# Performance work log

Measured on AMD Instinct MI355X. Metric: run time of the kernel, lower is better.

Reference implementation:

```python
import jax, jax.numpy as jnp
import numpy as np

B, U1, U2 = 4, 2048, 2048
C = 256      # in_feat_dim
F = 256      # feat_dim
M = 4        # num_modes
D = C // M   # attention_mode_dim = 64
ATTN_CLIP = 500.0
LN_EPS = 1e-12


def setup_inputs() -> dict:
    key = jax.random.key(0)
    ks = jax.random.split(key, 8)
    s = 0.02  # base_initializer_range
    inp = {
        "query_feat": jax.random.normal(ks[0], (B, U1, C), jnp.float32),
        "key_feat": jax.random.normal(ks[1], (B, U2, C), jnp.float32),
        "Wq": jax.random.normal(ks[2], (M * D, C), jnp.float32) * s,
        "bq": jnp.zeros((M * D,), jnp.float32),
    }
    # tie_qk_scheme='shared': key linear shares query weights
    inp["Wk"] = inp["Wq"]
    inp["bk"] = inp["bq"]
    inp["Wv"] = jax.random.normal(ks[3], (M * F, C), jnp.float32) * s  # first_linear, v_has_bias=False
    inp["W_mid"] = jax.random.normal(ks[4], (F, F), jnp.float32) * s   # MMSharedMid shared_linear
    inp["b_mid"] = jnp.zeros((F,), jnp.float32)
    inp["W_out"] = jax.random.normal(ks[5], (M, F, F), jnp.float32) * s  # grouped 1x1 conv, per mode
    inp["b_out"] = jnp.zeros((M, F), jnp.float32)
    inp["ln_g"] = jnp.ones((F,), jnp.float32)   # resout LayerNorm
    inp["ln_b"] = jnp.zeros((F,), jnp.float32)
    inp["W_score"] = jax.random.normal(ks[6], (1, F), jnp.float32) * s  # LearnedSoftAggregate
    inp["b_score"] = jnp.zeros((1,), jnp.float32)
    return inp


def _layer_norm(x, g, b):
    mu = jnp.mean(x, axis=-1, keepdims=True)
    var = jnp.var(x, axis=-1, keepdims=True)
    return (x - mu) * jax.lax.rsqrt(var + LN_EPS) * g + b


def reference(query_feat, key_feat, Wq, bq, Wk, bk, Wv, W_mid, b_mid,
              W_out, b_out, ln_g, ln_b, W_score, b_score):
    # --- tied-QK multi-mode attention ---
    q = (query_feat @ Wq.T + bq).reshape(B, U1, M, D)
    k = (key_feat @ Wk.T + bk).reshape(B, U2, M, D)
    scores = jnp.einsum('bimd,bjmd->bmij', q, k) / jnp.sqrt(jnp.float32(D))
    scores = jnp.clip(scores, -ATTN_CLIP, ATTN_CLIP)  # attn_clip
    probs = jax.nn.softmax(scores, axis=-1)           # [B, M, U1, U2]

    # --- ExpandedFeatTrans: value projection + fusion ---
    v = (key_feat @ Wv.T).reshape(B, U2, M, F)        # first_linear (no bias)
    fused = jnp.einsum('bmij,bjmf->bmif', probs, v)   # [B, M, U1, F]

    # MMSharedMid: shared linear over F + gelu (dropout = identity in eval)
    mid = jax.nn.gelu(fused @ W_mid.T + b_mid, approximate=False)

    # MMPrivateOutput: per-mode grouped 1x1 conv; NOTE the original code computes
    # x_comb = x + shortcut but then layer-norms x (shortcut dropped) - kept faithful.
    out = jnp.einsum('bmif,mgf->bmig', mid, W_out) + b_out[None, :, None, :]
    out = _layer_norm(out, ln_g, ln_b)                # [B, M, U1, F]

    # LearnedSoftAggregate over modes (group_dim=1, keepdim=False)
    mode_scores = out @ W_score.T + b_score           # [B, M, U1, 1]
    mode_probs = jax.nn.softmax(mode_scores, axis=1)
    return jnp.sum(out * mode_probs, axis=1)          # [B, U1, F]
```

## Files before the change

kernel.cpp:

```cpp
#include <hip/hip_runtime.h>

typedef __attribute__((ext_vector_type(8))) short short8;
typedef __attribute__((ext_vector_type(4))) float f32x4;
typedef __attribute__((ext_vector_type(16))) float f32x16;
typedef unsigned short u16t;
typedef unsigned int u32t;

#define MFMA16(a, b, c) __builtin_amdgcn_mfma_f32_16x16x32_bf16((a), (b), (c), 0, 0, 0)
#define MFMA32(a, b, c) __builtin_amdgcn_mfma_f32_32x32x16_bf16((a), (b), (c), 0, 0, 0)

__device__ __forceinline__ u16t f2bf(float f) {
  u32t u = __float_as_uint(f);
  u32t r = u + 0x7fffu + ((u >> 16) & 1u);
  return (u16t)(r >> 16);
}
__device__ __forceinline__ float bf2f(u16t b) {
  return __uint_as_float(((u32t)b) << 16);
}
__device__ __forceinline__ short8 pack8(float4 a0, float4 a1) {
  short8 r;
  r[0] = (short)f2bf(a0.x); r[1] = (short)f2bf(a0.y);
  r[2] = (short)f2bf(a0.z); r[3] = (short)f2bf(a0.w);
  r[4] = (short)f2bf(a1.x); r[5] = (short)f2bf(a1.y);
  r[6] = (short)f2bf(a1.z); r[7] = (short)f2bf(a1.w);
  return r;
}
__device__ __forceinline__ u32t packrhu(float a, float b) {
  u32t ua = __float_as_uint(a) + 0x8000u;
  u32t ub = __float_as_uint(b) + 0x8000u;
  return (ua >> 16) | (ub & 0xffff0000u);
}

__device__ __forceinline__ void proj_dev(
    const float* __restrict__ A, const float* __restrict__ W,
    const float* __restrict__ bias, float scale,
    u16t* __restrict__ out, int mode, int bx, int by,
    u16t* As, u16t* Ws) {
  const int tid = threadIdx.x;
  const int w = tid >> 6, lane = tid & 63, quad = lane >> 4, l15 = lane & 15;
  const int l31 = lane & 31, h8 = (lane >> 5) * 8;
  const int rt = bx * 64;
  const int ct = by * 64;
  const int wrow = (w >> 1) * 32, wcol = (w & 1) * 32;
  const int r2 = tid >> 3, c8 = tid & 7;

  const f32x4 fzero = {0.f, 0.f, 0.f, 0.f};
  f32x4 acc[2][2];
#pragma unroll
  for (int i = 0; i < 2; i++)
#pragma unroll
    for (int j = 0; j < 2; j++) acc[i][j] = fzero;

  for (int kt = 0; kt < 4; ++kt) {
    __syncthreads();
#pragma unroll
    for (int hh = 0; hh < 2; ++hh) {
      int rr = r2 + hh * 32;
      const float4* pa = (const float4*)(A + (size_t)(rt + rr) * 256 + kt * 64 + c8 * 8);
      const float4* pw = (const float4*)(W + (size_t)(ct + rr) * 256 + kt * 64 + c8 * 8);
      float4 w0 = pw[0], w1 = pw[1];
      w0.x *= scale; w0.y *= scale; w0.z *= scale; w0.w *= scale;
      w1.x *= scale; w1.y *= scale; w1.z *= scale; w1.w *= scale;
      *(short8*)&As[rr * 72 + c8 * 8] = pack8(pa[0], pa[1]);
      *(short8*)&Ws[rr * 72 + c8 * 8] = pack8(w0, w1);
    }
    __syncthreads();
#pragma unroll
    for (int ks = 0; ks < 2; ++ks) {
      short8 af0 = *(const short8*)&As[(wrow + l15) * 72 + ks * 32 + quad * 8];
      short8 af1 = *(const short8*)&As[(wrow + 16 + l15) * 72 + ks * 32 + quad * 8];
      short8 bw0 = *(const short8*)&Ws[(wcol + l15) * 72 + ks * 32 + quad * 8];
      short8 bw1 = *(const short8*)&Ws[(wcol + 16 + l15) * 72 + ks * 32 + quad * 8];
      acc[0][0] = MFMA16(af0, bw0, acc[0][0]);
      acc[0][1] = MFMA16(af0, bw1, acc[0][1]);
      acc[1][0] = MFMA16(af1, bw0, acc[1][0]);
      acc[1][1] = MFMA16(af1, bw1, acc[1][1]);
    }
  }

  __syncthreads();
  u16t* Cs = As;
  if (mode == 0) {
#pragma unroll
    for (int i = 0; i < 2; i++) {
      int rl = wrow + i * 16 + quad * 4;
#pragma unroll
      for (int j = 0; j < 2; j++) {
        int cl = wcol + j * 16 + l15;
        float bv = bias ? bias[ct + cl] * scale : 0.f;
#pragma unroll
        for (int rg = 0; rg < 4; ++rg)
          Cs[(rl + rg) * 72 + cl] = f2bf(acc[i][j][rg] + bv);
      }
    }
  } else {
#pragma unroll
    for (int i = 0; i < 2; i++) {
      int rl = wrow + i * 16 + quad * 4;
#pragma unroll
      for (int j = 0; j < 2; j++) {
        int cl = wcol + j * 16 + l15;
        ushort4 pk;
        pk.x = f2bf(acc[i][j][0]);
        pk.y = f2bf(acc[i][j][1]);
        pk.z = f2bf(acc[i][j][2]);
        pk.w = f2bf(acc[i][j][3]);
        *(ushort4*)&Cs[cl * 72 + rl] = pk;
      }
    }
  }
  __syncthreads();

#pragma unroll
  for (int t2 = 0; t2 < 2; ++t2) {
    short8 frag = *(const short8*)&Cs[(t2 * 32 + l31) * 72 + w * 16 + h8];
    size_t base;
    if (mode == 0) {
      int b = rt >> 11, m = by;
      int it32 = ((rt & 2047) >> 5) + t2;
      base = (((size_t)(b * 4 + m) * 64 + it32) * 4 + w) * 512;
    } else {
      int b = rt >> 11, m = by >> 2;
      int fb = ((by & 3) << 1) + t2;
      int jt16 = ((rt & 2047) >> 4) + w;
      base = (((size_t)(b * 4 + m) * 8 + fb) * 128 + jt16) * 512;
    }
    *(short8*)(out + base + lane * 8) = frag;
  }
}

__global__ __launch_bounds__(256) void prep_kernel(
    const float* __restrict__ query, const float* __restrict__ key,
    const float* __restrict__ Wq, const float* __restrict__ bq,
    const float* __restrict__ Wv, const float* __restrict__ Wm,
    const float* __restrict__ Wo,
    u16t* __restrict__ WmB, u16t* __restrict__ WoB,
    u16t* __restrict__ QfB, u16t* __restrict__ KfB, u16t* __restrict__ VfB) {
  __shared__ __align__(16) u16t As[64 * 72];
  __shared__ __align__(16) u16t Ws[64 * 72];
  const int blk = blockIdx.x;
  const int tid = threadIdx.x;
  if (blk < 256) {
    int i = blk * 256 + tid;
    WmB[i] = f2bf(Wm[i]);
    return;
  }
  if (blk < 1280) {
    int i = (blk - 256) * 256 + tid;
    WoB[i] = f2bf(Wo[i]);
    return;
  }
  const float *A, *W, *bias;
  float scale;
  u16t* out;
  int mode, local;
  if (blk < 1792) {
    local = blk - 1280; A = query; W = Wq; bias = bq; scale = 0.125f; out = QfB; mode = 0;
  } else if (blk < 2304) {
    local = blk - 1792; A = key; W = Wq; bias = bq; scale = 1.0f; out = KfB; mode = 0;
  } else {
    local = blk - 2304; A = key; W = Wv; bias = nullptr; scale = 1.0f; out = VfB; mode = 1;
  }
  proj_dev(A, W, bias, scale, out, mode, local & 127, local >> 7, As, Ws);
}

__global__ __launch_bounds__(256, 3) void attn_kernel(
    const u16t* __restrict__ Qf, const u16t* __restrict__ Kf,
    const u16t* __restrict__ Vf,
    const u16t* __restrict__ Wmid, const u16t* __restrict__ Wout,
    const float* __restrict__ b_mid, const float* __restrict__ b_out,
    const float* __restrict__ ln_g, const float* __restrict__ ln_b,
    const float* __restrict__ Wsc, const float* __restrict__ b_sc,
    u16t* __restrict__ out_ln, float* __restrict__ scoresWS) {
  __shared__ __align__(16) u16t smBig[16640];
  __shared__ float smL[128];
  __shared__ float smR[128];
  __shared__ float smS[64];
  const int tid = threadIdx.x;
  const int w = tid >> 6, lane = tid & 63, quad = lane >> 4, l15 = lane & 15;
  const int l31 = lane & 31, h = lane >> 5;
  const int L = blockIdx.x;
  const int xcd = L & 7, slot = L >> 3;
  const int bm = xcd * 2 + (slot >> 6);
  const int it32 = slot & 63;
  const int m = bm & 3;
  const int q0 = it32 * 32;

  const size_t lane8 = (size_t)lane * 8;

  const u16t* qbase = Qf + ((size_t)(bm * 64 + it32) * 4) * 512 + lane8;
  short8 qf4[4];
#pragma unroll
  for (int ksd = 0; ksd < 4; ++ksd)
    qf4[ksd] = *(const short8*)(qbase + ksd * 512);

  const u16t* kbase = Kf + ((size_t)bm * 256) * 512 + lane8;
  const u16t* vbase = Vf + ((size_t)(bm * 8 + 2 * w) * 128) * 512 + lane8;

  f32x16 facc[2];
#pragma unroll
  for (int j = 0; j < 2; j++)
#pragma unroll
    for (int r = 0; r < 16; r++) facc[j][r] = 0.f;
  float lsum = 0.f;

  short8 kfA[4], kfB[4];
#pragma unroll
  for (int ksd = 0; ksd < 4; ++ksd) {
    kfA[ksd] = *(const short8*)(kbase + (size_t)w * 2048 + ksd * 512);
    kfB[ksd] = *(const short8*)(kbase + (size_t)(w + 4) * 2048 + ksd * 512);
  }

#pragma unroll 1
  for (int t = 0; t < 8; ++t) {
    u16t* Pb = &smBig[(t & 1) * 8320];
    f32x16 saccA, saccB;
#pragma unroll
    for (int r = 0; r < 16; r++) { saccA[r] = 0.f; saccB[r] = 0.f; }
#pragma unroll
    for (int ksd = 0; ksd < 4; ++ksd) {
      saccA = MFMA32(kfA[ksd], qf4[ksd], saccA);
      saccB = MFMA32(kfB[ksd], qf4[ksd], saccB);
    }

    float ls = 0.f;
#pragma unroll
    for (int tt = 0; tt < 8; ++tt) {
      const int jl = ((2 * tt) & 3) + 8 * ((2 * tt) >> 2) + 4 * h;
      float a0 = __expf(saccA[2 * tt]);
      float a1 = __expf(saccA[2 * tt + 1]);
      float b0 = __expf(saccB[2 * tt]);
      float b1 = __expf(saccB[2 * tt + 1]);
      ls += a0 + a1 + b0 + b1;
      *(u32t*)&Pb[l31 * 260 + w * 32 + jl] = packrhu(a0, a1);
      *(u32t*)&Pb[l31 * 260 + (w + 4) * 32 + jl] = packrhu(b0, b1);
    }
    lsum += ls;

    __syncthreads();

    if (t < 7) {
      const int jA = (t + 1) * 8 + w, jB = jA + 4;
#pragma unroll
      for (int ksd = 0; ksd < 4; ++ksd) {
        kfA[ksd] = *(const short8*)(kbase + (size_t)jA * 2048 + ksd * 512);
        kfB[ksd] = *(const short8*)(kbase + (size_t)jB * 2048 + ksd * 512);
      }
    }
#pragma unroll
    for (int jj = 0; jj < 8; ++jj) {
      short8 vf[2][2];
#pragma unroll
      for (int fb = 0; fb < 2; ++fb)
#pragma unroll
        for (int ks2 = 0; ks2 < 2; ++ks2)
          vf[fb][ks2] = *(const short8*)(vbase + ((size_t)fb * 128 + (t * 16 + jj * 2 + ks2)) * 512);
      short8 bbL[2];
#pragma unroll
      for (int ks2 = 0; ks2 < 2; ++ks2)
        bbL[ks2] = *(const short8*)&Pb[l31 * 260 + jj * 32 + ks2 * 16 + h * 8];
      facc[0] = MFMA32(vf[0][0], bbL[0], facc[0]);
      facc[0] = MFMA32(vf[0][1], bbL[1], facc[0]);
      facc[1] = MFMA32(vf[1][0], bbL[0], facc[1]);
      facc[1] = MFMA32(vf[1][1], bbL[1], facc[1]);
    }
  }

  lsum += __shfl_xor(lsum, 32);
  if (h == 0) smL[w * 32 + l31] = lsum;
  __syncthreads();
  float inv = 1.f / (smL[l31] + smL[32 + l31] + smL[64 + l31] + smL[96 + l31]);

  u16t* smF = smBig;
#pragma unroll
  for (int fb = 0; fb < 2; ++fb) {
#pragma unroll
    for (int g = 0; g < 4; ++g) {
      int fbase = w * 64 + fb * 32 + 8 * g + 4 * h;
      ushort4 pk4;
      pk4.x = f2bf(facc[fb][4 * g + 0] * inv);
      pk4.y = f2bf(facc[fb][4 * g + 1] * inv);
      pk4.z = f2bf(facc[fb][4 * g + 2] * inv);
      pk4.w = f2bf(facc[fb][4 * g + 3] * inv);
      *(ushort4*)&smF[l31 * 264 + fbase] = pk4;
    }
  }
  __syncthreads();

  const int rgrp = w >> 1, ch = w & 1;
  const int rowq = rgrp * 16 + quad * 4;
  const f32x4 fz4 = {0.f, 0.f, 0.f, 0.f};

  f32x4 macc[8];
#pragma unroll
  for (int i = 0; i < 8; i++) macc[i] = fz4;
  for (int kc = 0; kc < 8; ++kc) {
    short8 af = *(const short8*)&smF[(rgrp * 16 + l15) * 264 + kc * 32 + quad * 8];
#pragma unroll
    for (int nb = 0; nb < 8; ++nb) {
      short8 bw = *(const short8*)(Wmid + (size_t)(ch * 128 + nb * 16 + l15) * 256 + kc * 32 + quad * 8);
      macc[nb] = MFMA16(af, bw, macc[nb]);
    }
  }
#pragma unroll
  for (int nb = 0; nb < 8; ++nb) {
    int c = ch * 128 + nb * 16 + l15;
    float bmv = b_mid[c];
#pragma unroll
    for (int rg = 0; rg < 4; ++rg) {
      float x = macc[nb][rg] + bmv;
      macc[nb][rg] = 0.5f * x * (1.f + erff(x * 0.70710678118654752f));
    }
  }
  __syncthreads();
#pragma unroll
  for (int nb = 0; nb < 8; ++nb)
#pragma unroll
    for (int rg = 0; rg < 4; ++rg)
      smF[(rowq + rg) * 264 + ch * 128 + nb * 16 + l15] = f2bf(macc[nb][rg]);
  __syncthreads();

  const u16t* Wo = Wout + (size_t)m * 65536;
  f32x4 oacc[8];
#pragma unroll
  for (int i = 0; i < 8; i++) oacc[i] = fz4;
  for (int kc = 0; kc < 8; ++kc) {
    short8 af = *(const short8*)&smF[(rgrp * 16 + l15) * 264 + kc * 32 + quad * 8];
#pragma unroll
    for (int nb = 0; nb < 8; ++nb) {
      short8 bw = *(const short8*)(Wo + (size_t)(ch * 128 + nb * 16 + l15) * 256 + kc * 32 + quad * 8);
      oacc[nb] = MFMA16(af, bw, oacc[nb]);
    }
  }

  float sum[4] = {0, 0, 0, 0}, sq[4] = {0, 0, 0, 0};
#pragma unroll
  for (int nb = 0; nb < 8; ++nb) {
    int c = ch * 128 + nb * 16 + l15;
    float bo = b_out[m * 256 + c];
#pragma unroll
    for (int rg = 0; rg < 4; ++rg) {
      float x = oacc[nb][rg] + bo;
      oacc[nb][rg] = x;
      sum[rg] += x;
      sq[rg] += x * x;
    }
  }
#pragma unroll
  for (int rg = 0; rg < 4; ++rg) {
    float s = sum[rg], s2 = sq[rg];
    s += __shfl_xor(s, 1); s += __shfl_xor(s, 2); s += __shfl_xor(s, 4); s += __shfl_xor(s, 8);
    s2 += __shfl_xor(s2, 1); s2 += __shfl_xor(s2, 2); s2 += __shfl_xor(s2, 4); s2 += __shfl_xor(s2, 8);
    if (l15 == 0) {
      smR[(rowq + rg) + 32 * ch] = s;
      smR[64 + (rowq + rg) + 32 * ch] = s2;
    }
  }
  __syncthreads();
  float mu[4], rstd[4];
#pragma unroll
  for (int rg = 0; rg < 4; ++rg) {
    int r = rowq + rg;
    float s = smR[r] + smR[r + 32];
    float s2 = smR[64 + r] + smR[64 + r + 32];
    float mean = s * (1.f / 256.f);
    float var = s2 * (1.f / 256.f) - mean * mean;
    mu[rg] = mean;
    rstd[rg] = rsqrtf(var + 1e-12f);
  }

  float scp[4] = {0, 0, 0, 0};
#pragma unroll
  for (int nb = 0; nb < 8; ++nb) {
    int c = ch * 128 + nb * 16 + l15;
    float g = ln_g[c], bb2 = ln_b[c], wsv = Wsc[c];
#pragma unroll
    for (int rg = 0; rg < 4; ++rg) {
      float xn = (oacc[nb][rg] - mu[rg]) * rstd[rg] * g + bb2;
      out_ln[((size_t)bm * 2048 + (q0 + rowq + rg)) * 256 + c] = f2bf(xn);
      scp[rg] += xn * wsv;
    }
  }
#pragma unroll
  for (int rg = 0; rg < 4; ++rg) {
    float s = scp[rg];
    s += __shfl_xor(s, 1); s += __shfl_xor(s, 2); s += __shfl_xor(s, 4); s += __shfl_xor(s, 8);
    if (l15 == 0) smS[(rowq + rg) + 32 * ch] = s;
  }
  __syncthreads();
  if (ch == 0 && l15 == 0) {
#pragma unroll
    for (int rg = 0; rg < 4; ++rg) {
      int r = rowq + rg;
      scoresWS[bm * 2048 + q0 + r] = smS[r] + smS[r + 32] + b_sc[0];
    }
  }
}

__global__ __launch_bounds__(256) void agg_kernel(
    const u16t* __restrict__ out_ln, const float* __restrict__ scoresWS,
    float* __restrict__ out) {
  const int row = blockIdx.x;
  const int c = threadIdx.x;
  const int b = row >> 11, i = row & 2047;
  float s0 = scoresWS[(b * 4 + 0) * 2048 + i];
  float s1 = scoresWS[(b * 4 + 1) * 2048 + i];
  float s2 = scoresWS[(b * 4 + 2) * 2048 + i];
  float s3 = scoresWS[(b * 4 + 3) * 2048 + i];
  float mx = fmaxf(fmaxf(s0, s1), fmaxf(s2, s3));
  float e0 = __expf(s0 - mx), e1 = __expf(s1 - mx), e2 = __expf(s2 - mx), e3 = __expf(s3 - mx);
  float inv = 1.f / (e0 + e1 + e2 + e3);
  float acc = e0 * inv * bf2f(out_ln[((size_t)(b * 4 + 0) * 2048 + i) * 256 + c]) +
              e1 * inv * bf2f(out_ln[((size_t)(b * 4 + 1) * 2048 + i) * 256 + c]) +
              e2 * inv * bf2f(out_ln[((size_t)(b * 4 + 2) * 2048 + i) * 256 + c]) +
              e3 * inv * bf2f(out_ln[((size_t)(b * 4 + 3) * 2048 + i) * 256 + c]);
  out[(size_t)row * 256 + c] = acc;
}

extern "C" void kernel_launch(void* const* d_in, const int* in_sizes, int n_in,
                              void* d_out, int out_size, void* d_ws, size_t ws_size,
                              hipStream_t stream) {
  (void)in_sizes; (void)n_in; (void)out_size; (void)ws_size;
  const float* query = (const float*)d_in[0];
  const float* key   = (const float*)d_in[1];
  const float* Wq    = (const float*)d_in[2];
  const float* bq    = (const float*)d_in[3];
  const float* Wv    = (const float*)d_in[6];
  const float* Wm    = (const float*)d_in[7];
  const float* bmid  = (const float*)d_in[8];
  const float* Wo    = (const float*)d_in[9];
  const float* bo    = (const float*)d_in[10];
  const float* lng   = (const float*)d_in[11];
  const float* lnb   = (const float*)d_in[12];
  const float* Wsc   = (const float*)d_in[13];
  const float* bsc   = (const float*)d_in[14];

  char* p = (char*)d_ws;
  u16t* QfB = (u16t*)p; p += (size_t)2097152 * 2;
  u16t* KfB = (u16t*)p; p += (size_t)2097152 * 2;
  u16t* VfB = (u16t*)p; p += (size_t)8388608 * 2;
  u16t* WmB = (u16t*)p; p += (size_t)65536 * 2;
  u16t* WoB = (u16t*)p; p += (size_t)262144 * 2;
  u16t* outLn = (u16t*)p; p += (size_t)8388608 * 2;
  float* scWS = (float*)p; p += (size_t)32768 * 4;

  prep_kernel<<<4352, 256, 0, stream>>>(query, key, Wq, bq, Wv, Wm, Wo,
                                        WmB, WoB, QfB, KfB, VfB);

  attn_kernel<<<1024, 256, 0, stream>>>(QfB, KfB, VfB, WmB, WoB,
                                        bmid, bo, lng, lnb, Wsc, bsc,
                                        outLn, scWS);

  agg_kernel<<<8192, 256, 0, stream>>>(outLn, scWS, (float*)d_out);
}
```

Before: 247.1 us.

## Double attention query tile to 64 rows per block to reuse K/V loads

Each attention block now processes 64 query rows (two 32-row sub-tiles) instead of 32, so every K and V fragment loaded from global memory feeds twice as many MFMAs. The grid is halved to 512 blocks, each with 16 key steps of 4 key blocks, and the per-sub-tile softmax sums are tracked separately. The MLP/LayerNorm tail is re-partitioned so each wave owns 16 full rows, which removes the shared-memory reductions and two barriers for row statistics and scores. The cost is more accumulator registers, since the launch-bounds occupancy hint is dropped, and only 512 blocks, which risks lower occupancy and latency hiding.

After: 281.5 us. 1.14x slower.

```diff
diff --git a/kernel.cpp b/kernel.cpp
--- a/kernel.cpp
+++ b/kernel.cpp
@@ -164,7 +164,7 @@
   proj_dev(A, W, bias, scale, out, mode, local & 127, local >> 7, As, Ws);
 }
 
-__global__ __launch_bounds__(256, 3) void attn_kernel(
+__global__ __launch_bounds__(256) void attn_kernel(
     const u16t* __restrict__ Qf, const u16t* __restrict__ Kf,
     const u16t* __restrict__ Vf,
     const u16t* __restrict__ Wmid, const u16t* __restrict__ Wout,
@@ -172,139 +172,145 @@
     const float* __restrict__ ln_g, const float* __restrict__ ln_b,
     const float* __restrict__ Wsc, const float* __restrict__ b_sc,
     u16t* __restrict__ out_ln, float* __restrict__ scoresWS) {
-  __shared__ __align__(16) u16t smBig[16640];
-  __shared__ float smL[128];
-  __shared__ float smR[128];
-  __shared__ float smS[64];
+  __shared__ __align__(16) u16t smBig[16896];
+  __shared__ float smL[256];
   const int tid = threadIdx.x;
   const int w = tid >> 6, lane = tid & 63, quad = lane >> 4, l15 = lane & 15;
   const int l31 = lane & 31, h = lane >> 5;
   const int L = blockIdx.x;
   const int xcd = L & 7, slot = L >> 3;
-  const int bm = xcd * 2 + (slot >> 6);
-  const int it32 = slot & 63;
+  const int bm = xcd * 2 + (slot >> 5);
+  const int it64 = slot & 31;
   const int m = bm & 3;
-  const int q0 = it32 * 32;
+  const int q0 = it64 * 64;
 
   const size_t lane8 = (size_t)lane * 8;
 
-  const u16t* qbase = Qf + ((size_t)(bm * 64 + it32) * 4) * 512 + lane8;
-  short8 qf4[4];
-#pragma unroll
-  for (int ksd = 0; ksd < 4; ++ksd)
-    qf4[ksd] = *(const short8*)(qbase + ksd * 512);
+  const u16t* qb0 = Qf + ((size_t)(bm * 64 + it64 * 2) * 4) * 512 + lane8;
+  short8 qf[2][4];
+#pragma unroll
+  for (int ib = 0; ib < 2; ++ib)
+#pragma unroll
+    for (int ksd = 0; ksd < 4; ++ksd)
+      qf[ib][ksd] = *(const short8*)(qb0 + ((size_t)ib * 4 + ksd) * 512);
 
   const u16t* kbase = Kf + ((size_t)bm * 256) * 512 + lane8;
   const u16t* vbase = Vf + ((size_t)(bm * 8 + 2 * w) * 128) * 512 + lane8;
 
-  f32x16 facc[2];
-#pragma unroll
-  for (int j = 0; j < 2; j++)
-#pragma unroll
-    for (int r = 0; r < 16; r++) facc[j][r] = 0.f;
-  float lsum = 0.f;
-
-  short8 kfA[4], kfB[4];
-#pragma unroll
-  for (int ksd = 0; ksd < 4; ++ksd) {
-    kfA[ksd] = *(const short8*)(kbase + (size_t)w * 2048 + ksd * 512);
-    kfB[ksd] = *(const short8*)(kbase + (size_t)(w + 4) * 2048 + ksd * 512);
-  }
+  f32x16 facc[2][2];
+#pragma unroll
+  for (int a = 0; a < 2; a++)
+#pragma unroll
+    for (int b2 = 0; b2 < 2; b2++)
+#pragma unroll
+      for (int r = 0; r < 16; r++) facc[a][b2][r] = 0.f;
+  float lsum[2] = {0.f, 0.f};
+
+  short8 kf4[4];
+#pragma unroll
+  for (int ksd = 0; ksd < 4; ++ksd)
+    kf4[ksd] = *(const short8*)(kbase + (size_t)w * 2048 + ksd * 512);
 
 #pragma unroll 1
-  for (int t = 0; t < 8; ++t) {
-    u16t* Pb = &smBig[(t & 1) * 8320];
-    f32x16 saccA, saccB;
-#pragma unroll
-    for (int r = 0; r < 16; r++) { saccA[r] = 0.f; saccB[r] = 0.f; }
-#pragma unroll
-    for (int ksd = 0; ksd < 4; ++ksd) {
-      saccA = MFMA32(kfA[ksd], qf4[ksd], saccA);
-      saccB = MFMA32(kfB[ksd], qf4[ksd], saccB);
-    }
-
-    float ls = 0.f;
-#pragma unroll
-    for (int tt = 0; tt < 8; ++tt) {
-      const int jl = ((2 * tt) & 3) + 8 * ((2 * tt) >> 2) + 4 * h;
-      float a0 = __expf(saccA[2 * tt]);
-      float a1 = __expf(saccA[2 * tt + 1]);
-      float b0 = __expf(saccB[2 * tt]);
-      float b1 = __expf(saccB[2 * tt + 1]);
-      ls += a0 + a1 + b0 + b1;
-      *(u32t*)&Pb[l31 * 260 + w * 32 + jl] = packrhu(a0, a1);
-      *(u32t*)&Pb[l31 * 260 + (w + 4) * 32 + jl] = packrhu(b0, b1);
-    }
-    lsum += ls;
+  for (int t = 0; t < 16; ++t) {
+    u16t* Pb = &smBig[(t & 1) * 8448];
+#pragma unroll
+    for (int ib = 0; ib < 2; ++ib) {
+      f32x16 sacc;
+#pragma unroll
+      for (int r = 0; r < 16; r++) sacc[r] = 0.f;
+#pragma unroll
+      for (int ksd = 0; ksd < 4; ++ksd)
+        sacc = MFMA32(kf4[ksd], qf[ib][ksd], sacc);
+      float ls = 0.f;
+#pragma unroll
+      for (int tt = 0; tt < 8; ++tt) {
+        const int jl = ((2 * tt) & 3) + 8 * ((2 * tt) >> 2) + 4 * h;
+        float p0 = __expf(sacc[2 * tt]);
+        float p1 = __expf(sacc[2 * tt + 1]);
+        ls += p0 + p1;
+        *(u32t*)&Pb[ib * 4224 + l31 * 132 + w * 32 + jl] = packrhu(p0, p1);
+      }
+      lsum[ib] += ls;
+    }
 
     __syncthreads();
 
-    if (t < 7) {
-      const int jA = (t + 1) * 8 + w, jB = jA + 4;
-#pragma unroll
-      for (int ksd = 0; ksd < 4; ++ksd) {
-        kfA[ksd] = *(const short8*)(kbase + (size_t)jA * 2048 + ksd * 512);
-        kfB[ksd] = *(const short8*)(kbase + (size_t)jB * 2048 + ksd * 512);
+    if (t < 15) {
+      const int jn = (t + 1) * 4 + w;
+#pragma unroll
+      for (int ksd = 0; ksd < 4; ++ksd)
+        kf4[ksd] = *(const short8*)(kbase + (size_t)jn * 2048 + ksd * 512);
+    }
+#pragma unroll
+    for (int jj = 0; jj < 4; ++jj) {
+      short8 vf[2][2];
+#pragma unroll
+      for (int fb = 0; fb < 2; ++fb)
+#pragma unroll
+        for (int ks2 = 0; ks2 < 2; ++ks2)
+          vf[fb][ks2] = *(const short8*)(vbase + ((size_t)fb * 128 + (t * 8 + jj * 2 + ks2)) * 512);
+#pragma unroll
+      for (int ib = 0; ib < 2; ++ib) {
+        short8 bbL[2];
+#pragma unroll
+        for (int ks2 = 0; ks2 < 2; ++ks2)
+          bbL[ks2] = *(const short8*)&Pb[ib * 4224 + l31 * 132 + jj * 32 + ks2 * 16 + h * 8];
+        facc[0][ib] = MFMA32(vf[0][0], bbL[0], facc[0][ib]);
+        facc[0][ib] = MFMA32(vf[0][1], bbL[1], facc[0][ib]);
+        facc[1][ib] = MFMA32(vf[1][0], bbL[0], facc[1][ib]);
+        facc[1][ib] = MFMA32(vf[1][1], bbL[1], facc[1][ib]);
       }
     }
-#pragma unroll
-    for (int jj = 0; jj < 8; ++jj) {
-      short8 vf[2][2];
-#pragma unroll
-      for (int fb = 0; fb < 2; ++fb)
-#pragma unroll
-        for (int ks2 = 0; ks2 < 2; ++ks2)
-          vf[fb][ks2] = *(const short8*)(vbase + ((size_t)fb * 128 + (t * 16 + jj * 2 + ks2)) * 512);
-      short8 bbL[2];
-#pragma unroll
-      for (int ks2 = 0; ks2 < 2; ++ks2)
-        bbL[ks2] = *(const short8*)&Pb[l31 * 260 + jj * 32 + ks2 * 16 + h * 8];
-      facc[0] = MFMA32(vf[0][0], bbL[0], facc[0]);
-      facc[0] = MFMA32(vf[0][1], bbL[1], facc[0]);
-      facc[1] = MFMA32(vf[1][0], bbL[0], facc[1]);
-      facc[1] = MFMA32(vf[1][1], bbL[1], facc[1]);
-    }
-  }
-
-  lsum += __shfl_xor(lsum, 32);
-  if (h == 0) smL[w * 32 + l31] = lsum;
-  __syncthreads();
-  float inv = 1.f / (smL[l31] + smL[32 + l31] + smL[64 + l31] + smL[96 + l31]);
+  }
+
+#pragma unroll
+  for (int ib = 0; ib < 2; ++ib) {
+    lsum[ib] += __shfl_xor(lsum[ib], 32);
+    if (h == 0) smL[ib * 128 + w * 32 + l31] = lsum[ib];
+  }
+  __syncthreads();
+  float inv[2];
+#pragma unroll
+  for (int ib = 0; ib < 2; ++ib)
+    inv[ib] = 1.f / (smL[ib * 128 + l31] + smL[ib * 128 + 32 + l31] +
+                     smL[ib * 128 + 64 + l31] + smL[ib * 128 + 96 + l31]);
 
   u16t* smF = smBig;
 #pragma unroll
-  for (int fb = 0; fb < 2; ++fb) {
-#pragma unroll
-    for (int g = 0; g < 4; ++g) {
-      int fbase = w * 64 + fb * 32 + 8 * g + 4 * h;
-      ushort4 pk4;
-      pk4.x = f2bf(facc[fb][4 * g + 0] * inv);
-      pk4.y = f2bf(facc[fb][4 * g + 1] * inv);
-      pk4.z = f2bf(facc[fb][4 * g + 2] * inv);
-      pk4.w = f2bf(facc[fb][4 * g + 3] * inv);
-      *(ushort4*)&smF[l31 * 264 + fbase] = pk4;
-    }
-  }
-  __syncthreads();
-
-  const int rgrp = w >> 1, ch = w & 1;
-  const int rowq = rgrp * 16 + quad * 4;
+  for (int fb = 0; fb < 2; ++fb)
+#pragma unroll
+    for (int ib = 0; ib < 2; ++ib) {
+      const int i = ib * 32 + l31;
+#pragma unroll
+      for (int g = 0; g < 4; ++g) {
+        int fbase = w * 64 + fb * 32 + 8 * g + 4 * h;
+        ushort4 pk4;
+        pk4.x = f2bf(facc[fb][ib][4 * g + 0] * inv[ib]);
+        pk4.y = f2bf(facc[fb][ib][4 * g + 1] * inv[ib]);
+        pk4.z = f2bf(facc[fb][ib][4 * g + 2] * inv[ib]);
+        pk4.w = f2bf(facc[fb][ib][4 * g + 3] * inv[ib]);
+        *(ushort4*)&smF[i * 264 + fbase] = pk4;
+      }
+    }
+  __syncthreads();
+
   const f32x4 fz4 = {0.f, 0.f, 0.f, 0.f};
 
-  f32x4 macc[8];
-#pragma unroll
-  for (int i = 0; i < 8; i++) macc[i] = fz4;
+  f32x4 macc[16];
+#pragma unroll
+  for (int i = 0; i < 16; i++) macc[i] = fz4;
   for (int kc = 0; kc < 8; ++kc) {
-    short8 af = *(const short8*)&smF[(rgrp * 16 + l15) * 264 + kc * 32 + quad * 8];
-#pragma unroll
-    for (int nb = 0; nb < 8; ++nb) {
-      short8 bw = *(const short8*)(Wmid + (size_t)(ch * 128 + nb * 16 + l15) * 256 + kc * 32 + quad * 8);
+    short8 af = *(const short8*)&smF[(16 * w + l15) * 264 + kc * 32 + quad * 8];
+#pragma unroll
+    for (int nb = 0; nb < 16; ++nb) {
+      short8 bw = *(const short8*)(Wmid + (size_t)(nb * 16 + l15) * 256 + kc * 32 + quad * 8);
       macc[nb] = MFMA16(af, bw, macc[nb]);
     }
   }
 #pragma unroll
-  for (int nb = 0; nb < 8; ++nb) {
-    int c = ch * 128 + nb * 16 + l15;
+  for (int nb = 0; nb < 16; ++nb) {
+    int c = nb * 16 + l15;
     float bmv = b_mid[c];
 #pragma unroll
     for (int rg = 0; rg < 4; ++rg) {
@@ -314,29 +320,29 @@
   }
   __syncthreads();
 #pragma unroll
-  for (int nb = 0; nb < 8; ++nb)
+  for (int nb = 0; nb < 16; ++nb)
 #pragma unroll
     for (int rg = 0; rg < 4; ++rg)
-      smF[(rowq + rg) * 264 + ch * 128 + nb * 16 + l15] = f2bf(macc[nb][rg]);
+      smF[(16 * w + quad * 4 + rg) * 264 + nb * 16 + l15] = f2bf(macc[nb][rg]);
   __syncthreads();
 
   const u16t* Wo = Wout + (size_t)m * 65536;
-  f32x4 oacc[8];
-#pragma unroll
-  for (int i = 0; i < 8; i++) oacc[i] = fz4;
+  f32x4 oacc[16];
+#pragma unroll
+  for (int i = 0; i < 16; i++) oacc[i] = fz4;
   for (int kc = 0; kc < 8; ++kc) {
-    short8 af = *(const short8*)&smF[(rgrp * 16 + l15) * 264 + kc * 32 + quad * 8];
-#pragma unroll
-    for (int nb = 0; nb < 8; ++nb) {
-      short8 bw = *(const short8*)(Wo + (size_t)(ch * 128 + nb * 16 + l15) * 256 + kc * 32 + quad * 8);
+    short8 af = *(const short8*)&smF[(16 * w + l15) * 264 + kc * 32 + quad * 8];
+#pragma unroll
+    for (int nb = 0; nb < 16; ++nb) {
+      short8 bw = *(const short8*)(Wo + (size_t)(nb * 16 + l15) * 256 + kc * 32 + quad * 8);
       oacc[nb] = MFMA16(af, bw, oacc[nb]);
     }
   }
 
   float sum[4] = {0, 0, 0, 0}, sq[4] = {0, 0, 0, 0};
 #pragma unroll
-  for (int nb = 0; nb < 8; ++nb) {
-    int c = ch * 128 + nb * 16 + l15;
+  for (int nb = 0; nb < 16; ++nb) {
+    int c = nb * 16 + l15;
     float bo = b_out[m * 256 + c];
 #pragma unroll
     for (int rg = 0; rg < 4; ++rg) {
@@ -346,23 +352,12 @@
       sq[rg] += x * x;
     }
   }
+  float mu[4], rstd[4];
 #pragma unroll
   for (int rg = 0; rg < 4; ++rg) {
     float s = sum[rg], s2 = sq[rg];
     s += __shfl_xor(s, 1); s += __shfl_xor(s, 2); s += __shfl_xor(s, 4); s += __shfl_xor(s, 8);
     s2 += __shfl_xor(s2, 1); s2 += __shfl_xor(s2, 2); s2 += __shfl_xor(s2, 4); s2 += __shfl_xor(s2, 8);
-    if (l15 == 0) {
-      smR[(rowq + rg) + 32 * ch] = s;
-      smR[64 + (rowq + rg) + 32 * ch] = s2;
-    }
-  }
-  __syncthreads();
-  float mu[4], rstd[4];
-#pragma unroll
-  for (int rg = 0; rg < 4; ++rg) {
-    int r = rowq + rg;
-    float s = smR[r] + smR[r + 32];
-    float s2 = smR[64 + r] + smR[64 + r + 32];
     float mean = s * (1.f / 256.f);
     float var = s2 * (1.f / 256.f) - mean * mean;
     mu[rg] = mean;
@@ -371,13 +366,13 @@
 
   float scp[4] = {0, 0, 0, 0};
 #pragma unroll
-  for (int nb = 0; nb < 8; ++nb) {
-    int c = ch * 128 + nb * 16 + l15;
+  for (int nb = 0; nb < 16; ++nb) {
+    int c = nb * 16 + l15;
     float g = ln_g[c], bb2 = ln_b[c], wsv = Wsc[c];
 #pragma unroll
     for (int rg = 0; rg < 4; ++rg) {
       float xn = (oacc[nb][rg] - mu[rg]) * rstd[rg] * g + bb2;
-      out_ln[((size_t)bm * 2048 + (q0 + rowq + rg)) * 256 + c] = f2bf(xn);
+      out_ln[((size_t)bm * 2048 + (q0 + 16 * w + quad * 4 + rg)) * 256 + c] = f2bf(xn);
       scp[rg] += xn * wsv;
     }
   }
@@ -385,15 +380,8 @@
   for (int rg = 0; rg < 4; ++rg) {
     float s = scp[rg];
     s += __shfl_xor(s, 1); s += __shfl_xor(s, 2); s += __shfl_xor(s, 4); s += __shfl_xor(s, 8);
-    if (l15 == 0) smS[(rowq + rg) + 32 * ch] = s;
-  }
-  __syncthreads();
-  if (ch == 0 && l15 == 0) {
-#pragma unroll
-    for (int rg = 0; rg < 4; ++rg) {
-      int r = rowq + rg;
-      scoresWS[bm * 2048 + q0 + r] = smS[r] + smS[r + 32] + b_sc[0];
-    }
+    if (l15 == 0)
+      scoresWS[bm * 2048 + q0 + 16 * w + quad * 4 + rg] = s + b_sc[0];
   }
 }
 
@@ -447,9 +435,9 @@
   prep_kernel<<<4352, 256, 0, stream>>>(query, key, Wq, bq, Wv, Wm, Wo,
                                         WmB, WoB, QfB, KfB, VfB);
 
-  attn_kernel<<<1024, 256, 0, stream>>>(QfB, KfB, VfB, WmB, WoB,
-                                        bmid, bo, lng, lnb, Wsc, bsc,
-                                        outLn, scWS);
+  attn_kernel<<<512, 256, 0, stream>>>(QfB, KfB, VfB, WmB, WoB,
+                                       bmid, bo, lng, lnb, Wsc, bsc,
+                                       outLn, scWS);
 
   agg_kernel<<<8192, 256, 0, stream>>>(outLn, scWS, (float*)d_out);
 }
```

## Software-pipeline QK scores one tile ahead of PV accumulation with smaller tiles

Applied to the files above, without the earlier changes.

Restructures the attention loop so each iteration computes the next 128-key score tile (exp, write to a double-buffered P tile) while running PV MFMAs on the current tile. Key tiles shrink from 256 to 128, so the iteration count doubles, and the shared-memory P buffers are split out from the F staging buffer. The aim is to overlap exp/score work with PV MFMAs and to cut LDS and register use. In exchange it needs twice as many barriers, with one at the end of every iteration.

Measured after the change: 235.5 us. 4.7% less time.

```diff
diff --git a/kernel.cpp b/kernel.cpp
--- a/kernel.cpp
+++ b/kernel.cpp
@@ -172,7 +172,8 @@
     const float* __restrict__ ln_g, const float* __restrict__ ln_b,
     const float* __restrict__ Wsc, const float* __restrict__ b_sc,
     u16t* __restrict__ out_ln, float* __restrict__ scoresWS) {
-  __shared__ __align__(16) u16t smBig[16640];
+  __shared__ __align__(16) u16t smF[32 * 264];
+  __shared__ __align__(16) u16t smP[2][32 * 132];
   __shared__ float smL[128];
   __shared__ float smR[128];
   __shared__ float smS[64];
@@ -204,66 +205,81 @@
     for (int r = 0; r < 16; r++) facc[j][r] = 0.f;
   float lsum = 0.f;
 
-  short8 kfA[4], kfB[4];
-#pragma unroll
-  for (int ksd = 0; ksd < 4; ++ksd) {
-    kfA[ksd] = *(const short8*)(kbase + (size_t)w * 2048 + ksd * 512);
-    kfB[ksd] = *(const short8*)(kbase + (size_t)(w + 4) * 2048 + ksd * 512);
-  }
-
-#pragma unroll 1
-  for (int t = 0; t < 8; ++t) {
-    u16t* Pb = &smBig[(t & 1) * 8320];
-    f32x16 saccA, saccB;
-#pragma unroll
-    for (int r = 0; r < 16; r++) { saccA[r] = 0.f; saccB[r] = 0.f; }
-#pragma unroll
-    for (int ksd = 0; ksd < 4; ++ksd) {
-      saccA = MFMA32(kfA[ksd], qf4[ksd], saccA);
-      saccB = MFMA32(kfB[ksd], qf4[ksd], saccB);
-    }
-
+  short8 kf4[4];
+#pragma unroll
+  for (int ksd = 0; ksd < 4; ++ksd)
+    kf4[ksd] = *(const short8*)(kbase + (size_t)w * 2048 + ksd * 512);
+
+  {
+    f32x16 sacc;
+#pragma unroll
+    for (int r = 0; r < 16; r++) sacc[r] = 0.f;
+#pragma unroll
+    for (int ksd = 0; ksd < 4; ++ksd)
+      sacc = MFMA32(kf4[ksd], qf4[ksd], sacc);
     float ls = 0.f;
 #pragma unroll
     for (int tt = 0; tt < 8; ++tt) {
       const int jl = ((2 * tt) & 3) + 8 * ((2 * tt) >> 2) + 4 * h;
-      float a0 = __expf(saccA[2 * tt]);
-      float a1 = __expf(saccA[2 * tt + 1]);
-      float b0 = __expf(saccB[2 * tt]);
-      float b1 = __expf(saccB[2 * tt + 1]);
-      ls += a0 + a1 + b0 + b1;
-      *(u32t*)&Pb[l31 * 260 + w * 32 + jl] = packrhu(a0, a1);
-      *(u32t*)&Pb[l31 * 260 + (w + 4) * 32 + jl] = packrhu(b0, b1);
+      float p0 = __expf(sacc[2 * tt]);
+      float p1 = __expf(sacc[2 * tt + 1]);
+      ls += p0 + p1;
+      *(u32t*)&smP[0][l31 * 132 + w * 32 + jl] = packrhu(p0, p1);
     }
     lsum += ls;
-
-    __syncthreads();
-
-    if (t < 7) {
-      const int jA = (t + 1) * 8 + w, jB = jA + 4;
-#pragma unroll
-      for (int ksd = 0; ksd < 4; ++ksd) {
-        kfA[ksd] = *(const short8*)(kbase + (size_t)jA * 2048 + ksd * 512);
-        kfB[ksd] = *(const short8*)(kbase + (size_t)jB * 2048 + ksd * 512);
+  }
+#pragma unroll
+  for (int ksd = 0; ksd < 4; ++ksd)
+    kf4[ksd] = *(const short8*)(kbase + (size_t)(4 + w) * 2048 + ksd * 512);
+  __syncthreads();
+
+#pragma unroll 1
+  for (int t = 0; t < 16; ++t) {
+    u16t* Pb = &smP[t & 1][0];
+    u16t* Pn = &smP[(t + 1) & 1][0];
+
+    if (t < 15) {
+      f32x16 sacc;
+#pragma unroll
+      for (int r = 0; r < 16; r++) sacc[r] = 0.f;
+#pragma unroll
+      for (int ksd = 0; ksd < 4; ++ksd)
+        sacc = MFMA32(kf4[ksd], qf4[ksd], sacc);
+      float ls = 0.f;
+#pragma unroll
+      for (int tt = 0; tt < 8; ++tt) {
+        const int jl = ((2 * tt) & 3) + 8 * ((2 * tt) >> 2) + 4 * h;
+        float p0 = __expf(sacc[2 * tt]);
+        float p1 = __expf(sacc[2 * tt + 1]);
+        ls += p0 + p1;
+        *(u32t*)&Pn[l31 * 132 + w * 32 + jl] = packrhu(p0, p1);
       }
-    }
-#pragma unroll
-    for (int jj = 0; jj < 8; ++jj) {
+      lsum += ls;
+    }
+    if (t < 14) {
+      const int jn = (t + 2) * 4 + w;
+#pragma unroll
+      for (int ksd = 0; ksd < 4; ++ksd)
+        kf4[ksd] = *(const short8*)(kbase + (size_t)jn * 2048 + ksd * 512);
+    }
+#pragma unroll
+    for (int jj = 0; jj < 4; ++jj) {
       short8 vf[2][2];
 #pragma unroll
       for (int fb = 0; fb < 2; ++fb)
 #pragma unroll
         for (int ks2 = 0; ks2 < 2; ++ks2)
-          vf[fb][ks2] = *(const short8*)(vbase + ((size_t)fb * 128 + (t * 16 + jj * 2 + ks2)) * 512);
+          vf[fb][ks2] = *(const short8*)(vbase + ((size_t)fb * 128 + (t * 8 + jj * 2 + ks2)) * 512);
       short8 bbL[2];
 #pragma unroll
       for (int ks2 = 0; ks2 < 2; ++ks2)
-        bbL[ks2] = *(const short8*)&Pb[l31 * 260 + jj * 32 + ks2 * 16 + h * 8];
+        bbL[ks2] = *(const short8*)&Pb[l31 * 132 + jj * 32 + ks2 * 16 + h * 8];
       facc[0] = MFMA32(vf[0][0], bbL[0], facc[0]);
       facc[0] = MFMA32(vf[0][1], bbL[1], facc[0]);
       facc[1] = MFMA32(vf[1][0], bbL[0], facc[1]);
       facc[1] = MFMA32(vf[1][1], bbL[1], facc[1]);
     }
+    __syncthreads();
   }
 
   lsum += __shfl_xor(lsum, 32);
@@ -271,7 +287,6 @@
   __syncthreads();
   float inv = 1.f / (smL[l31] + smL[32 + l31] + smL[64 + l31] + smL[96 + l31]);
 
-  u16t* smF = smBig;
 #pragma unroll
   for (int fb = 0; fb < 2; ++fb) {
 #pragma unroll
```
